# Kernel tuning notes

Hardware: AMD Instinct MI355X
Metric: run time of the kernel (lower is better)

Reference implementation:

```python
import jax, jax.numpy as jnp
import numpy as np

N = 50000       # n_nodes
E = 800000      # n_edges
DIN = 64
DH = 64
DOUT = 64


def setup_inputs() -> dict:
    key = jax.random.key(0)
    k0, k1, k2, k3, k4 = jax.random.split(key, 5)
    x = jax.random.normal(k0, (N, DIN), dtype=jnp.float32)
    edge_index = jax.random.randint(k1, (2, E), 0, N, dtype=jnp.int32)
    # learnable per-edge weight (nn.Parameter); positive init keeps gcn_norm well-defined
    edge_weight = jax.random.uniform(k2, (E,), jnp.float32, 0.1, 1.0)
    W1 = jax.random.normal(k3, (DH, DIN), dtype=jnp.float32) * (1.0 / np.sqrt(DIN))
    b1 = jnp.zeros((DH,), jnp.float32)
    W2 = jax.random.normal(k4, (DOUT, DH), dtype=jnp.float32) * (1.0 / np.sqrt(DH))
    b2 = jnp.zeros((DOUT,), jnp.float32)
    return {"x": x, "edge_weight": edge_weight, "W1": W1, "b1": b1,
            "W2": W2, "b2": b2, "edge_index": edge_index}


def _gcn_norm(edge_index, edge_weight, n):
    # PyG gcn_norm: add self-loops (weight 1), symmetric normalization.
    loop = jnp.arange(n, dtype=edge_index.dtype)
    row = jnp.concatenate([edge_index[0], loop])   # source nodes
    col = jnp.concatenate([edge_index[1], loop])   # target nodes
    w = jnp.concatenate([edge_weight, jnp.ones((n,), edge_weight.dtype)])
    deg = jax.ops.segment_sum(w, col, num_segments=n)
    dinv = jnp.where(deg > 0, jax.lax.rsqrt(jnp.where(deg > 0, deg, 1.0)), 0.0)
    norm = dinv[row] * w * dinv[col]               # [E + N]
    return row, col, norm


def _gcn_layer(x, W, b, row, col, norm, n):
    h = x @ W.T                                     # [N, out]
    # gather source features, scale by norm, scatter-add into targets
    out = jax.ops.segment_sum(h[row] * norm[:, None], col, num_segments=n)
    return out + b


def reference(x, edge_weight, W1, b1, W2, b2, edge_index):
    n = x.shape[0]
    row, col, norm = _gcn_norm(edge_index, edge_weight, n)
    h = _gcn_layer(x, W1, b1, row, col, norm, n)
    h = jax.nn.relu(h)                              # self.pre: ReLU + Dropout (identity in eval)
    return _gcn_layer(h, W2, b2, row, col, norm, n)
```

## Files before the change

kernel.cpp:

```cpp
#include <hip/hip_runtime.h>

#define D 64
#define GN 128
#define SW 68
#define SX 132
#define MAXDEG 64
#define RBITS 8
#define RANGE 256
#define MAXB 5120
#define APB 2048

typedef unsigned long long u64;
typedef unsigned int u32;
typedef unsigned short u16;
typedef unsigned char u8;

__device__ __forceinline__ float4 fma4(float4 w, float s, float4 c) {
    c.x = fmaf(w.x, s, c.x); c.y = fmaf(w.y, s, c.y);
    c.z = fmaf(w.z, s, c.z); c.w = fmaf(w.w, s, c.w);
    return c;
}

__device__ __forceinline__ u32 f2bf(float f) {
    u32 u = __float_as_uint(f);
    return (u + 0x7FFFu + ((u >> 16) & 1u)) >> 16;
}
__device__ __forceinline__ u32 pack2(float a, float b) { return f2bf(a) | (f2bf(b) << 16); }
__device__ __forceinline__ float blo(u32 u) { return __uint_as_float(u << 16); }
__device__ __forceinline__ float bhi(u32 u) { return __uint_as_float(u & 0xFFFF0000u); }

__device__ __forceinline__ float decdeg(u64 dc) {
    return (float)(u32)dc * (1.0f / 16777216.0f) + 1.0f;
}

__global__ __launch_bounds__(256) void k_bucket(
        const int* __restrict__ ei, const float* __restrict__ ew,
        u64* __restrict__ barr, u32* __restrict__ gcount, int E, int NB) {
    __shared__ u64 srec[APB];
    __shared__ u8  sbkt[APB];
    __shared__ u32 scnt[256];
    __shared__ u32 sbase[256];

    int t = threadIdx.x;
    int e0 = blockIdx.x * APB;
    int ne = min(APB, E - e0);

    for (int i = t; i < 256; i += 256) scnt[i] = 0;
    __syncthreads();

    for (int i = t; i < ne; i += 256) {
        int e   = e0 + i;
        int r   = ei[e];
        int c   = ei[(size_t)E + e];
        float w = ew[e];
        int b   = c >> RBITS;
        srec[i] = ((u64)__float_as_uint(w) << 32)
                | (u32)r | ((u32)(c & (RANGE - 1)) << 20);
        sbkt[i] = (u8)b;
        atomicAdd(&scnt[b], 1u);
    }
    __syncthreads();

    for (int i = t; i < NB; i += 256) {
        u32 cnt = scnt[i];
        sbase[i] = cnt ? atomicAdd(&gcount[i], cnt) : 0u;
        scnt[i] = 0;
    }
    __syncthreads();

    for (int i = t; i < ne; i += 256) {
        int b   = sbkt[i];
        u32 rk  = atomicAdd(&scnt[b], 1u);
        u32 pos = sbase[b] + rk;
        if (pos < MAXB) barr[(size_t)b * MAXB + pos] = srec[i];
    }
}

__global__ __launch_bounds__(256) void k_scatter(
        const u64* __restrict__ barr, const u32* __restrict__ gcount,
        u64* __restrict__ degcnt, int2* __restrict__ eg) {
    int b    = blockIdx.x >> 1;
    int half = blockIdx.x & 1;
    u32 cnt  = min(gcount[b], (u32)MAXB);
    u32 h0   = (cnt + 1) >> 1;
    u32 beg  = half ? h0 : 0;
    u32 end  = half ? cnt : h0;
    int base_c = b << RBITS;

    for (u32 i = beg + threadIdx.x; i < end; i += 256) {
        u64 rec = barr[(size_t)b * MAXB + i];
        int src = (int)(rec & 0xFFFFFu);
        int c   = base_c + (int)((rec >> 20) & 0xFFu);
        u32 wb  = (u32)(rec >> 32);
        float w = __uint_as_float(wb);
        u64 packed = (1ULL << 32) | (u64)(u32)(w * 16777216.0f);
        u64 old = atomicAdd(&degcnt[c], packed);
        u32 rank = (u32)(old >> 32);
        if (rank < MAXDEG)
            eg[((size_t)c << 6) + rank] = make_int2(src, (int)wb);
    }
}

__global__ __launch_bounds__(256) void k_dinv(u64* __restrict__ degcnt, int N) {
    int n = blockIdx.x * 256 + threadIdx.x;
    if (n < N) {
        u64 dc = degcnt[n];
        float di = rsqrtf(decdeg(dc));
        degcnt[n] = (dc & 0xFFFFFFFF00000000ULL) | (u64)__float_as_uint(di);
    }
}

template<bool RELU_IN>
__global__ __launch_bounds__(256) void k_gemm(
        const float* __restrict__ in, const float* __restrict__ W,
        u16* __restrict__ h, int N) {
    __shared__ __align__(16) float sWt[D * SW];
    __shared__ __align__(16) float sxT[D * SX];

    int t = threadIdx.x;
    int node0 = blockIdx.x * GN;

    for (int i = t; i < D * D / 4; i += 256) {
        int j = i >> 4, k4 = i & 15;
        float4 w = ((const float4*)W)[i];
        sWt[(4 * k4 + 0) * SW + j] = w.x;
        sWt[(4 * k4 + 1) * SW + j] = w.y;
        sWt[(4 * k4 + 2) * SW + j] = w.z;
        sWt[(4 * k4 + 3) * SW + j] = w.w;
    }
    for (int i = t; i < GN * D / 4; i += 256) {
        int nn = i >> 4, k4 = i & 15;
        int n = node0 + nn;
        float4 v = make_float4(0.f, 0.f, 0.f, 0.f);
        if (n < N) v = ((const float4*)(in + (size_t)n * D))[k4];
        if (RELU_IN) {
            v.x = fmaxf(v.x, 0.f); v.y = fmaxf(v.y, 0.f);
            v.z = fmaxf(v.z, 0.f); v.w = fmaxf(v.w, 0.f);
        }
        sxT[(4 * k4 + 0) * SX + nn] = v.x;
        sxT[(4 * k4 + 1) * SX + nn] = v.y;
        sxT[(4 * k4 + 2) * SX + nn] = v.z;
        sxT[(4 * k4 + 3) * SX + nn] = v.w;
    }
    __syncthreads();

    int jg = (t & 7) * 8;
    int ng = (t >> 3) * 4;
    float4 a0[4], a1[4];
    #pragma unroll
    for (int a = 0; a < 4; ++a) {
        a0[a] = make_float4(0.f, 0.f, 0.f, 0.f);
        a1[a] = make_float4(0.f, 0.f, 0.f, 0.f);
    }

    #pragma unroll 8
    for (int k = 0; k < D; ++k) {
        const float* wr = &sWt[k * SW + jg];
        float4 w0 = *(const float4*)wr;
        float4 w1 = *(const float4*)(wr + 4);
        float4 xv = *(const float4*)&sxT[k * SX + ng];
        a0[0] = fma4(w0, xv.x, a0[0]);  a1[0] = fma4(w1, xv.x, a1[0]);
        a0[1] = fma4(w0, xv.y, a0[1]);  a1[1] = fma4(w1, xv.y, a1[1]);
        a0[2] = fma4(w0, xv.z, a0[2]);  a1[2] = fma4(w1, xv.z, a1[2]);
        a0[3] = fma4(w0, xv.w, a0[3]);  a1[3] = fma4(w1, xv.w, a1[3]);
    }

    #pragma unroll
    for (int a = 0; a < 4; ++a) {
        int n = node0 + ng + a;
        if (n >= N) continue;
        uint4 st;
        st.x = pack2(a0[a].x, a0[a].y);
        st.y = pack2(a0[a].z, a0[a].w);
        st.z = pack2(a1[a].x, a1[a].y);
        st.w = pack2(a1[a].z, a1[a].w);
        *(uint4*)(h + (size_t)n * D + jg) = st;
    }
}

__global__ __launch_bounds__(256) void k_aggregate(
        const u16* __restrict__ h, const u64* __restrict__ degcnt,
        const int2* __restrict__ eg, const float* __restrict__ b,
        float* __restrict__ out, int N) {
    int t = threadIdx.x;
    int n = blockIdx.x * 4 + (t >> 6);
    if (n >= N) return;
    int lane = t & 63;
    int g = lane >> 3;
    int f = (lane & 7) * 8;

    const u32* dv = (const u32*)degcnt;

    u64 dcn = degcnt[n];
    int c = min((int)(dcn >> 32), MAXDEG);
    float dinv_n = __uint_as_float((u32)dcn);

    float acc[8] = {0.f, 0.f, 0.f, 0.f, 0.f, 0.f, 0.f, 0.f};
    if (g == 0) {
        float d2 = dinv_n * dinv_n;
        uint4 hv = *(const uint4*)(h + ((size_t)n << 6) + f);
        float4 b0 = *(const float4*)(b + f);
        float4 b1 = *(const float4*)(b + f + 4);
        acc[0] = fmaf(blo(hv.x), d2, b0.x); acc[1] = fmaf(bhi(hv.x), d2, b0.y);
        acc[2] = fmaf(blo(hv.y), d2, b0.z); acc[3] = fmaf(bhi(hv.y), d2, b0.w);
        acc[4] = fmaf(blo(hv.z), d2, b1.x); acc[5] = fmaf(bhi(hv.z), d2, b1.y);
        acc[6] = fmaf(blo(hv.w), d2, b1.z); acc[7] = fmaf(bhi(hv.w), d2, b1.w);
    }

    size_t s = (size_t)n << 6;
    int i = g;
    for (; i + 8 < c; i += 16) {
        int2 e0 = eg[s + i];
        int2 e1 = eg[s + i + 8];
        float di0 = __uint_as_float(dv[(size_t)e0.x << 1]);
        float di1 = __uint_as_float(dv[(size_t)e1.x << 1]);
        uint4 h0 = *(const uint4*)(h + ((size_t)e0.x << 6) + f);
        uint4 h1 = *(const uint4*)(h + ((size_t)e1.x << 6) + f);
        float w0 = __int_as_float(e0.y) * dinv_n * di0;
        float w1 = __int_as_float(e1.y) * dinv_n * di1;
        acc[0] = fmaf(blo(h0.x), w0, acc[0]); acc[1] = fmaf(bhi(h0.x), w0, acc[1]);
        acc[2] = fmaf(blo(h0.y), w0, acc[2]); acc[3] = fmaf(bhi(h0.y), w0, acc[3]);
        acc[4] = fmaf(blo(h0.z), w0, acc[4]); acc[5] = fmaf(bhi(h0.z), w0, acc[5]);
        acc[6] = fmaf(blo(h0.w), w0, acc[6]); acc[7] = fmaf(bhi(h0.w), w0, acc[7]);
        acc[0] = fmaf(blo(h1.x), w1, acc[0]); acc[1] = fmaf(bhi(h1.x), w1, acc[1]);
        acc[2] = fmaf(blo(h1.y), w1, acc[2]); acc[3] = fmaf(bhi(h1.y), w1, acc[3]);
        acc[4] = fmaf(blo(h1.z), w1, acc[4]); acc[5] = fmaf(bhi(h1.z), w1, acc[5]);
        acc[6] = fmaf(blo(h1.w), w1, acc[6]); acc[7] = fmaf(bhi(h1.w), w1, acc[7]);
    }
    if (i < c) {
        int2 e0 = eg[s + i];
        float di0 = __uint_as_float(dv[(size_t)e0.x << 1]);
        uint4 h0 = *(const uint4*)(h + ((size_t)e0.x << 6) + f);
        float w0 = __int_as_float(e0.y) * dinv_n * di0;
        acc[0] = fmaf(blo(h0.x), w0, acc[0]); acc[1] = fmaf(bhi(h0.x), w0, acc[1]);
        acc[2] = fmaf(blo(h0.y), w0, acc[2]); acc[3] = fmaf(bhi(h0.y), w0, acc[3]);
        acc[4] = fmaf(blo(h0.z), w0, acc[4]); acc[5] = fmaf(bhi(h0.z), w0, acc[5]);
        acc[6] = fmaf(blo(h0.w), w0, acc[6]); acc[7] = fmaf(bhi(h0.w), w0, acc[7]);
    }

    #pragma unroll
    for (int k = 0; k < 8; ++k) {
        acc[k] += __shfl_xor(acc[k], 8);
        acc[k] += __shfl_xor(acc[k], 16);
        acc[k] += __shfl_xor(acc[k], 32);
    }

    if (g == 0) {
        float4* o = (float4*)(out + ((size_t)n << 6) + f);
        o[0] = make_float4(acc[0], acc[1], acc[2], acc[3]);
        o[1] = make_float4(acc[4], acc[5], acc[6], acc[7]);
    }
}

extern "C" void kernel_launch(void* const* d_in, const int* in_sizes, int n_in,
                              void* d_out, int out_size, void* d_ws, size_t ws_size,
                              hipStream_t stream) {
    const float* x  = (const float*)d_in[0];
    const float* ew = (const float*)d_in[1];
    const float* W1 = (const float*)d_in[2];
    const float* b1 = (const float*)d_in[3];
    const float* W2 = (const float*)d_in[4];
    const float* b2 = (const float*)d_in[5];
    const int*   ei = (const int*)d_in[6];

    int N = in_sizes[0] / D;
    int E = in_sizes[1];
    int NB = (N + RANGE - 1) >> RBITS;
    float* out = (float*)d_out;

    char* p = (char*)d_ws;
    u64*   degcnt = (u64*)p;   p += (size_t)N * 8;
    int2*  eg     = (int2*)p;  p += (size_t)N * MAXDEG * 8;
    u16*   h      = (u16*)p;   p += (size_t)N * D * 2;
    float* agg1   = (float*)p; p += (size_t)N * D * 4;
    u64*   barr   = (u64*)agg1;
    u32*   gcount = (u32*)((char*)agg1 + 12 * 1024 * 1024);

    dim3 blk(256);
    int gemm_grid   = (N + GN - 1) / GN;
    int bucket_grid = (E + APB - 1) / APB;
    int agg_grid    = (N + 3) / 4;

    hipMemsetAsync(degcnt, 0, (size_t)N * 8, stream);
    hipMemsetAsync(gcount, 0, 4096, stream);

    k_bucket<<<dim3(bucket_grid), blk, 0, stream>>>(ei, ew, barr, gcount, E, NB);
    k_scatter<<<dim3(2 * NB), blk, 0, stream>>>(barr, gcount, degcnt, eg);
    k_dinv<<<dim3((N + 255) / 256), blk, 0, stream>>>(degcnt, N);

    k_gemm<false><<<dim3(gemm_grid), blk, 0, stream>>>(x, W1, h, N);
    k_aggregate<<<dim3(agg_grid), blk, 0, stream>>>(h, degcnt, eg, b1, agg1, N);

    k_gemm<true><<<dim3(gemm_grid), blk, 0, stream>>>(agg1, W2, h, N);
    k_aggregate<<<dim3(agg_grid), blk, 0, stream>>>(h, degcnt, eg, b2, out, N);
}
```

Measured before the change: 198.2 us.

## Build per-bucket adjacency in shared memory and fuse degree normalization into scatter

The scatter kernel now runs one block per 256-node bucket and builds that bucket's neighbor lists, counts and weighted degrees with shared-memory atomics, then writes dinv and the padded edge list out with coalesced int4 stores. This removes the global 64-bit atomics, the degcnt memset and the separate dinv kernel. The aggregate inner loop is also turned into a fully unrolled 8-step predicated loop. The cost is a 128KB shared buffer per block, which allows only one block per CU and halves the grid of the scatter stage. The scatter also copies every padded slot, including unused ones.

```diff
diff --git a/kernel.cpp b/kernel.cpp
--- a/kernel.cpp
+++ b/kernel.cpp
@@ -28,10 +28,6 @@
 __device__ __forceinline__ u32 pack2(float a, float b) { return f2bf(a) | (f2bf(b) << 16); }
 __device__ __forceinline__ float blo(u32 u) { return __uint_as_float(u << 16); }
 __device__ __forceinline__ float bhi(u32 u) { return __uint_as_float(u & 0xFFFF0000u); }
-
-__device__ __forceinline__ float decdeg(u64 dc) {
-    return (float)(u32)dc * (1.0f / 16777216.0f) + 1.0f;
-}
 
 __global__ __launch_bounds__(256) void k_bucket(
         const int* __restrict__ ei, const float* __restrict__ ew,
@@ -76,38 +72,46 @@
     }
 }
 
-__global__ __launch_bounds__(256) void k_scatter(
+__global__ __launch_bounds__(256, 1) void k_scatter(
         const u64* __restrict__ barr, const u32* __restrict__ gcount,
-        u64* __restrict__ degcnt, int2* __restrict__ eg) {
-    int b    = blockIdx.x >> 1;
-    int half = blockIdx.x & 1;
-    u32 cnt  = min(gcount[b], (u32)MAXB);
-    u32 h0   = (cnt + 1) >> 1;
-    u32 beg  = half ? h0 : 0;
-    u32 end  = half ? cnt : h0;
+        u64* __restrict__ degcnt, int2* __restrict__ eg, int N) {
+    __shared__ int2  seg[RANGE * MAXDEG];
+    __shared__ u32   scnt[RANGE];
+    __shared__ float sdeg[RANGE];
+
+    int b = blockIdx.x;
+    int t = threadIdx.x;
+    u32 cnt = min(gcount[b], (u32)MAXB);
     int base_c = b << RBITS;
 
-    for (u32 i = beg + threadIdx.x; i < end; i += 256) {
+    for (int i = t; i < RANGE; i += 256) { scnt[i] = 0; sdeg[i] = 1.0f; }
+    __syncthreads();
+
+    for (u32 i = t; i < cnt; i += 256) {
         u64 rec = barr[(size_t)b * MAXB + i];
         int src = (int)(rec & 0xFFFFFu);
-        int c   = base_c + (int)((rec >> 20) & 0xFFu);
+        int cl  = (int)((rec >> 20) & 0xFFu);
         u32 wb  = (u32)(rec >> 32);
-        float w = __uint_as_float(wb);
-        u64 packed = (1ULL << 32) | (u64)(u32)(w * 16777216.0f);
-        u64 old = atomicAdd(&degcnt[c], packed);
-        u32 rank = (u32)(old >> 32);
-        if (rank < MAXDEG)
-            eg[((size_t)c << 6) + rank] = make_int2(src, (int)wb);
-    }
-}
-
-__global__ __launch_bounds__(256) void k_dinv(u64* __restrict__ degcnt, int N) {
-    int n = blockIdx.x * 256 + threadIdx.x;
-    if (n < N) {
-        u64 dc = degcnt[n];
-        float di = rsqrtf(decdeg(dc));
-        degcnt[n] = (dc & 0xFFFFFFFF00000000ULL) | (u64)__float_as_uint(di);
-    }
+        u32 rank = atomicAdd(&scnt[cl], 1u);
+        atomicAdd(&sdeg[cl], __uint_as_float(wb));
+        if (rank < MAXDEG) seg[(cl << 6) + rank] = make_int2(src, (int)wb);
+    }
+    __syncthreads();
+
+    for (int i = t; i < RANGE; i += 256) {
+        int n = base_c + i;
+        if (n < N) {
+            u32 c2 = min(scnt[i], (u32)MAXDEG);
+            float di = rsqrtf(sdeg[i]);
+            degcnt[n] = ((u64)c2 << 32) | (u64)__float_as_uint(di);
+        }
+    }
+
+    int nt = min(RANGE, N - base_c);
+    const int4* s4 = (const int4*)seg;
+    int4* d4 = (int4*)(eg + ((size_t)base_c << 6));
+    int tot = nt << 5;
+    for (int i = t; i < tot; i += 256) d4[i] = s4[i];
 }
 
 template<bool RELU_IN>
@@ -208,34 +212,19 @@
     }
 
     size_t s = (size_t)n << 6;
-    int i = g;
-    for (; i + 8 < c; i += 16) {
-        int2 e0 = eg[s + i];
-        int2 e1 = eg[s + i + 8];
-        float di0 = __uint_as_float(dv[(size_t)e0.x << 1]);
-        float di1 = __uint_as_float(dv[(size_t)e1.x << 1]);
-        uint4 h0 = *(const uint4*)(h + ((size_t)e0.x << 6) + f);
-        uint4 h1 = *(const uint4*)(h + ((size_t)e1.x << 6) + f);
-        float w0 = __int_as_float(e0.y) * dinv_n * di0;
-        float w1 = __int_as_float(e1.y) * dinv_n * di1;
-        acc[0] = fmaf(blo(h0.x), w0, acc[0]); acc[1] = fmaf(bhi(h0.x), w0, acc[1]);
-        acc[2] = fmaf(blo(h0.y), w0, acc[2]); acc[3] = fmaf(bhi(h0.y), w0, acc[3]);
-        acc[4] = fmaf(blo(h0.z), w0, acc[4]); acc[5] = fmaf(bhi(h0.z), w0, acc[5]);
-        acc[6] = fmaf(blo(h0.w), w0, acc[6]); acc[7] = fmaf(bhi(h0.w), w0, acc[7]);
-        acc[0] = fmaf(blo(h1.x), w1, acc[0]); acc[1] = fmaf(bhi(h1.x), w1, acc[1]);
-        acc[2] = fmaf(blo(h1.y), w1, acc[2]); acc[3] = fmaf(bhi(h1.y), w1, acc[3]);
-        acc[4] = fmaf(blo(h1.z), w1, acc[4]); acc[5] = fmaf(bhi(h1.z), w1, acc[5]);
-        acc[6] = fmaf(blo(h1.w), w1, acc[6]); acc[7] = fmaf(bhi(h1.w), w1, acc[7]);
-    }
-    if (i < c) {
-        int2 e0 = eg[s + i];
-        float di0 = __uint_as_float(dv[(size_t)e0.x << 1]);
-        uint4 h0 = *(const uint4*)(h + ((size_t)e0.x << 6) + f);
-        float w0 = __int_as_float(e0.y) * dinv_n * di0;
-        acc[0] = fmaf(blo(h0.x), w0, acc[0]); acc[1] = fmaf(bhi(h0.x), w0, acc[1]);
-        acc[2] = fmaf(blo(h0.y), w0, acc[2]); acc[3] = fmaf(bhi(h0.y), w0, acc[3]);
-        acc[4] = fmaf(blo(h0.z), w0, acc[4]); acc[5] = fmaf(bhi(h0.z), w0, acc[5]);
-        acc[6] = fmaf(blo(h0.w), w0, acc[6]); acc[7] = fmaf(bhi(h0.w), w0, acc[7]);
+    #pragma unroll
+    for (int k = 0; k < 8; ++k) {
+        int e = g + (k << 3);
+        if (e < c) {
+            int2 e0 = eg[s + e];
+            float di = __uint_as_float(dv[(size_t)e0.x << 1]);
+            uint4 hv = *(const uint4*)(h + ((size_t)e0.x << 6) + f);
+            float w = __int_as_float(e0.y) * dinv_n * di;
+            acc[0] = fmaf(blo(hv.x), w, acc[0]); acc[1] = fmaf(bhi(hv.x), w, acc[1]);
+            acc[2] = fmaf(blo(hv.y), w, acc[2]); acc[3] = fmaf(bhi(hv.y), w, acc[3]);
+            acc[4] = fmaf(blo(hv.z), w, acc[4]); acc[5] = fmaf(bhi(hv.z), w, acc[5]);
+            acc[6] = fmaf(blo(hv.w), w, acc[6]); acc[7] = fmaf(bhi(hv.w), w, acc[7]);
+        }
     }
 
     #pragma unroll
@@ -281,12 +270,10 @@
     int bucket_grid = (E + APB - 1) / APB;
     int agg_grid    = (N + 3) / 4;
 
-    hipMemsetAsync(degcnt, 0, (size_t)N * 8, stream);
     hipMemsetAsync(gcount, 0, 4096, stream);
 
     k_bucket<<<dim3(bucket_grid), blk, 0, stream>>>(ei, ew, barr, gcount, E, NB);
-    k_scatter<<<dim3(2 * NB), blk, 0, stream>>>(barr, gcount, degcnt, eg);
-    k_dinv<<<dim3((N + 255) / 256), blk, 0, stream>>>(degcnt, N);
+    k_scatter<<<dim3(NB), blk, 0, stream>>>(barr, gcount, degcnt, eg, N);
 
     k_gemm<false><<<dim3(gemm_grid), blk, 0, stream>>>(x, W1, h, N);
     k_aggregate<<<dim3(agg_grid), blk, 0, stream>>>(h, degcnt, eg, b1, agg1, N);
```

New measurement: 185.4 us. -6.4%, faster.
